# Kernel tuning notes

Hardware: AMD Instinct MI355X
Metric: run time of the kernel (lower is better)

Reference implementation:

```python
import jax, jax.numpy as jnp
import numpy as np
import math

E = 65536        # neighbor pairs (edges)
NAT = 2048       # atoms
NRAD = 24        # radial basis size
ZETA = [1, 2, 3, 4]
NCOMP = len(ZETA) + 1  # radial components: one 2-body + one per zeta
RCUT = 6.0
NELEM = 94       # one-hot element encoding size
EMB = 16         # species embedding dim


def _tables():
    """Static lxlylz enumeration per zeta: triples with lx+ly+lz = n, n in 0..z,
    multinomial/binomial normalization and (-1)^n lambda sign."""
    f = np.vectorize(math.factorial)
    tabs = []
    for z in ZETA:
        L = []
        for n in range(z + 1):
            for lx in range(n + 1):
                for ly in range(n - lx + 1):
                    L.append((lx, ly, n - lx - ly))
        L = np.array(L, np.int64)              # [K,3]
        nsum = L.sum(1)                        # [K]
        fact_lxlylz = f(L[:, 0]) * f(L[:, 1]) * f(L[:, 2])
        # (nfact/fact_lxlylz) * z!/((z-n)! n!) = z! / ((z-n)! * lx!ly!lz!)
        fact_norm = math.factorial(z) / (f(z - nsum) * fact_lxlylz)
        lam = (-1.0) ** nsum
        tabs.append((jnp.asarray(L, jnp.float32),
                     jnp.asarray(fact_norm, jnp.float32),
                     jnp.asarray(lam, jnp.float32)))
    return tabs

TABS = _tables()


def _forward(rij, Wr1, br1, Wr2, br2, Ws1, bs1, Ws2, bs2,
             Wa1, ba1, Wa2, ba2, Wa3, ba3, first_atom_idx, species_idx):
    nat = species_idx.shape[0]
    r = jnp.linalg.norm(rij, axis=1)                       # [E]
    u = rij / r[:, None]                                   # [E,3] unit vectors
    fc = 0.5 * (jnp.cos(jnp.pi * jnp.minimum(r, RCUT) / RCUT) + 1.0)
    centers = jnp.linspace(0.0, RCUT, NRAD, dtype=jnp.float32)
    width = RCUT / NRAD
    basis = jnp.exp(-((r[:, None] - centers) ** 2) / (2.0 * width * width)) * fc[:, None]  # [E,NRAD]
    # learned radial functions -> [E, NRAD, NCOMP]
    h = jax.nn.silu(basis @ Wr1 + br1)
    radial = jax.nn.silu(h @ Wr2 + br2).reshape(-1, NRAD, NCOMP)
    seg = first_atom_idx
    # two-body descriptor
    feats = [jax.ops.segment_sum(radial[:, :, 0], seg, num_segments=nat)]  # [nat,NRAD]
    for iz, z in enumerate(ZETA):
        L, fnorm, lam = TABS[iz]
        # g_ij over lxlylz combos: prod of powers of unit-vector components
        g_ij = jnp.prod((u[:, None, :] + 1e-12) ** L[None, :, :], axis=-1) * fnorm  # [E,K]
        g = jnp.einsum('er,ek->erk', radial[:, :, iz + 1], g_ij)                    # [E,NRAD,K]
        gi = jax.ops.segment_sum(g, seg, num_segments=nat)                          # [nat,NRAD,K]
        g2 = gi * gi
        norm = 2.0 ** (1.0 - z)
        feats.append(jnp.sum(g2, axis=-1) * norm)          # lambda = +1
        feats.append(jnp.sum(g2 * lam, axis=-1) * norm)    # lambda = -1
    feat = jnp.concatenate(feats, axis=1)                  # [nat, NRAD*(1+2*nzeta)]
    # species embedding and correlation
    onehot = jax.nn.one_hot(species_idx, NELEM, dtype=feat.dtype)
    emb = jax.nn.silu(onehot @ Ws1 + bs1) @ Ws2 + bs2      # [nat,EMB]
    x = (feat[:, :, None] * emb[:, None, :]).reshape(nat, -1)  # [nat, F*EMB]
    h = jax.nn.silu(x @ Wa1 + ba1)
    h = jax.nn.silu(h @ Wa2 + ba2)
    e = h @ Wa3 + ba3                                      # [nat,1] atomic energies
    return jnp.sum(e)                                      # total energy


def setup_inputs() -> dict:
    key = jax.random.key(0)
    ks = jax.random.split(key, 12)
    def w(k, shp):
        return jax.random.normal(k, shp, jnp.float32) / np.float32(np.sqrt(shp[0]))
    F = NRAD * (1 + 2 * len(ZETA)) * EMB  # 3456
    return {
        "rij": jax.random.normal(ks[0], (E, 3), jnp.float32) * 2.0,
        "Wr1": w(ks[1], (NRAD, 64)), "br1": jnp.zeros((64,), jnp.float32),
        "Wr2": w(ks[2], (64, NCOMP * NRAD)), "br2": jnp.zeros((NCOMP * NRAD,), jnp.float32),
        "Ws1": w(ks[3], (NELEM, 32)), "bs1": jnp.zeros((32,), jnp.float32),
        "Ws2": w(ks[4], (32, EMB)), "bs2": jnp.zeros((EMB,), jnp.float32),
        "Wa1": w(ks[5], (F, 256)), "ba1": jnp.zeros((256,), jnp.float32),
        "Wa2": w(ks[6], (256, 128)), "ba2": jnp.zeros((128,), jnp.float32),
        "Wa3": w(ks[7], (128, 1)), "ba3": jnp.zeros((1,), jnp.float32),
        "first_atom_idx": jnp.sort(jax.random.randint(ks[8], (E,), 0, NAT)),
        "species_idx": jax.random.randint(ks[9], (NAT,), 0, NELEM),
    }


def reference(rij, Wr1, br1, Wr2, br2, Ws1, bs1, Ws2, bs2,
              Wa1, ba1, Wa2, ba2, Wa3, ba3, first_atom_idx, species_idx):
    return _forward(rij, Wr1, br1, Wr2, br2, Ws1, bs1, Ws2, bs2,
                    Wa1, ba1, Wa2, ba2, Wa3, ba3, first_atom_idx, species_idx)
```

## Files before the change

kernel.cpp:

```cpp
#include <hip/hip_runtime.h>
#include <math.h>

#define KTOT 69
#define NRADC 24
#define NFEAT 216
#define NELEMC 94
#define EMBC 16
#define H1C 256
#define H2C 128
#define CE 16
#define EPR 20
#define KGN 18
#define GSTR 84
#define GISTR 76

__device__ __constant__ int c_lx[KTOT] = {
  0,0,0,1,
  0,0,0,1,0,0,0,1,1,2,
  0,0,0,1,0,0,0,1,1,2,0,0,0,0,1,1,1,2,2,3,
  0,0,0,1,0,0,0,1,1,2,0,0,0,0,1,1,1,2,2,3,0,0,0,0,0,1,1,1,1,2,2,2,3,3,4};
__device__ __constant__ int c_ly[KTOT] = {
  0,0,1,0,
  0,0,1,0,0,1,2,0,1,0,
  0,0,1,0,0,1,2,0,1,0,0,1,2,3,0,1,2,0,1,0,
  0,0,1,0,0,1,2,0,1,0,0,1,2,3,0,1,2,0,1,0,0,1,2,3,4,0,1,2,3,0,1,2,0,1,0};
__device__ __constant__ int c_lz[KTOT] = {
  0,1,0,0,
  0,1,0,0,2,1,0,1,0,0,
  0,1,0,0,2,1,0,1,0,0,3,2,1,0,2,1,0,1,0,0,
  0,1,0,0,2,1,0,1,0,0,3,2,1,0,2,1,0,1,0,0,4,3,2,1,0,3,2,1,0,2,1,0,1,0,0};
__device__ __constant__ float c_fn[KTOT] = {
  1,1,1,1,
  1,2,2,2,1,2,1,2,2,1,
  1,3,3,3,3,6,3,6,6,3,1,3,3,1,3,6,3,3,3,1,
  1,4,4,4,6,12,6,12,12,6,4,12,12,4,12,24,12,12,12,4,
  1,4,6,4,1,4,12,12,4,6,12,6,4,4,1};
__device__ __constant__ float c_lam[KTOT] = {
  1,-1,-1,-1,
  1,-1,-1,-1,1,1,1,1,1,1,
  1,-1,-1,-1,1,1,1,1,1,1,-1,-1,-1,-1,-1,-1,-1,-1,-1,-1,
  1,-1,-1,-1,1,1,1,1,1,1,-1,-1,-1,-1,-1,-1,-1,-1,-1,-1,
  1,1,1,1,1,1,1,1,1,1,1,1,1,1,1};
__device__ __constant__ int c_k0[4] = {0,4,14,34};
__device__ __constant__ int c_kn[4] = {4,10,20,35};
__device__ __constant__ float c_zn[4] = {1.0f, 0.5f, 0.25f, 0.125f};
__device__ __constant__ int c_zidg[KGN] = {0, 1,1,1, 2,2,2,2,2, 3,3,3,3,3,3,3,3,3};

__device__ __forceinline__ float silu(float x) { return x / (1.0f + expf(-x)); }
__device__ __forceinline__ float4 silu4(float4 v) {
  v.x = silu(v.x); v.y = silu(v.y); v.z = silu(v.z); v.w = silu(v.w); return v;
}
__device__ __forceinline__ void fma4(float4& a, float s, const float4 w) {
  a.x += s * w.x; a.y += s * w.y; a.z += s * w.z; a.w += s * w.w;
}
__device__ __forceinline__ void fma44(float4& a, const float4 x, const float4 y) {
  a.x += x.x * y.x; a.y += x.y * y.y; a.z += x.z * y.z; a.w += x.w * y.w;
}
__device__ __forceinline__ float hsum4(const float4 v) { return (v.x + v.y) + (v.z + v.w); }
__device__ __forceinline__ float powsel(int l, float p, float p2, float p3, float p4) {
  float v = 1.0f;
  v = l >= 1 ? p : v;
  v = l >= 2 ? p2 : v;
  v = l >= 3 ? p3 : v;
  v = l >= 4 ? p4 : v;
  return v;
}

__global__ void k_bounds(const int* __restrict__ fai, int* __restrict__ bounds,
                         int E, int nat) {
  int e = blockIdx.x * blockDim.x + threadIdx.x;
  if (e >= E) return;
  int f = fai[e];
  int fp = (e == 0) ? -1 : fai[e - 1];
  for (int a = fp + 1; a <= f; ++a) bounds[a] = e;
  if (e == E - 1)
    for (int a = f + 1; a <= nat; ++a) bounds[a] = E;
}

template <int NQ>
__device__ __forceinline__ void edge_layer2(
    const float* __restrict__ s_h, const float* __restrict__ Wr2,
    const float* __restrict__ br2, float4* __restrict__ radial4,
    int e, int og, int eg, int E) {
  float4 acc[NQ];
  const float4* b2 = (const float4*)(br2 + og * 32);
  #pragma unroll
  for (int q = 0; q < NQ; ++q) acc[q] = b2[q];
  #pragma unroll 2
  for (int j = 0; j < 64; ++j) {
    float hv = s_h[e * 65 + j];
    const float4* w = (const float4*)(Wr2 + j * 120 + og * 32);
    #pragma unroll
    for (int q = 0; q < NQ; ++q) fma4(acc[q], hv, w[q]);
  }
  if (eg < E) {
    #pragma unroll
    for (int q = 0; q < NQ; ++q)
      radial4[(size_t)(og * 8 + q) * E + eg] = silu4(acc[q]);
  }
}

__global__ __launch_bounds__(256) void k_edge(
    const float* __restrict__ rij,
    const float* __restrict__ Wr1, const float* __restrict__ br1,
    const float* __restrict__ Wr2, const float* __restrict__ br2,
    float4* __restrict__ radial4, int E) {
  __shared__ float s_bas[64 * 25];
  __shared__ float s_h[64 * 65];
  const int tid = threadIdx.x;
  const int e = tid & 63;
  const int og = __builtin_amdgcn_readfirstlane(tid >> 6);
  const int eg = blockIdx.x * 64 + e;

  {
    float x = 0.0f, y = 0.0f, z = 0.0f;
    if (eg < E) { x = rij[eg * 3 + 0]; y = rij[eg * 3 + 1]; z = rij[eg * 3 + 2]; }
    float r = sqrtf(x * x + y * y + z * z);
    float rc = fminf(r, 6.0f);
    float fcv = (eg < E)
        ? 0.5f * (cosf(3.14159265358979323846f * rc * (1.0f / 6.0f)) + 1.0f)
        : 0.0f;
    #pragma unroll
    for (int t = 0; t < 6; ++t) {
      int m = og * 6 + t;
      float d = r - (6.0f / 23.0f) * (float)m;
      s_bas[e * 25 + m] = expf(-8.0f * d * d) * fcv;
    }
  }
  __syncthreads();

  {
    const float4* b1 = (const float4*)(br1 + og * 16);
    float4 acc[4] = {b1[0], b1[1], b1[2], b1[3]};
    #pragma unroll 4
    for (int m = 0; m < NRADC; ++m) {
      float b = s_bas[e * 25 + m];
      const float4* w = (const float4*)(Wr1 + m * 64 + og * 16);
      #pragma unroll
      for (int q = 0; q < 4; ++q) fma4(acc[q], b, w[q]);
    }
    #pragma unroll
    for (int q = 0; q < 4; ++q) {
      float4 v = silu4(acc[q]);
      float* dst = &s_h[e * 65 + og * 16 + 4 * q];
      dst[0] = v.x; dst[1] = v.y; dst[2] = v.z; dst[3] = v.w;
    }
  }
  __syncthreads();

  if (og < 3) edge_layer2<8>(s_h, Wr2, br2, radial4, e, og, eg, E);
  else        edge_layer2<6>(s_h, Wr2, br2, radial4, e, og, eg, E);
}

__global__ __launch_bounds__(256) void k_atom(
    const float* __restrict__ rij,
    const float4* __restrict__ radial4,
    const int* __restrict__ bounds,
    float* __restrict__ feat, int E) {
  const int a = blockIdx.x;
  const int tid = threadIdx.x;
  __shared__ __align__(16) float s_radT[120 * EPR];
  __shared__ __align__(16) float s_gijT[KGN * GSTR];
  __shared__ __align__(16) float s_gi[NRADC * GISTR];
  __shared__ float s_feat[NFEAT];

  const int start = bounds[a];
  const int end = bounds[a + 1];

  const bool is_tile = tid < 216;
  const int eh = is_tile ? (tid / 108) : 0;
  const int tile = is_tile ? (tid % 108) : 0;
  const int rg = tile % 6;
  const int kg = tile / 6;
  const int zz = c_zidg[kg];
  const int comp0 = rg * 20 + 1 + zz;
  const bool is_2b = (tid >= 216 && tid < 240);
  const int rad2b = tid - 216;

  if (tid < 60) {
    int rr = tid / EPR, e = tid % EPR;
    int fkg = rr < 2 ? 3 : 17;
    int fj = rr < 2 ? 2 + rr : 3;
    s_gijT[fkg * GSTR + fj * EPR + e] = 0.0f;
  }

  float4 acc[4][4];
  #pragma unroll
  for (int i = 0; i < 4; ++i)
    #pragma unroll
    for (int j = 0; j < 4; ++j) acc[i][j] = make_float4(0, 0, 0, 0);
  float4 acc2b = make_float4(0, 0, 0, 0);

  for (int c0 = start; c0 < end; c0 += CE) {
    const int ne = min(CE, end - c0);
    for (int idx = tid; idx < 30 * CE; idx += 256) {
      int o4 = idx >> 4;
      int e = idx & 15;
      float4 v = make_float4(0, 0, 0, 0);
      if (e < ne) v = radial4[(size_t)o4 * E + (c0 + e)];
      int c = o4 * 4;
      s_radT[(c + 0) * EPR + e] = v.x;
      s_radT[(c + 1) * EPR + e] = v.y;
      s_radT[(c + 2) * EPR + e] = v.z;
      s_radT[(c + 3) * EPR + e] = v.w;
    }
    {
      int e = tid >> 4, sub = tid & 15;
      int eg = c0 + e;
      bool ev = e < ne;
      float x = 1.0f, y = 0.0f, z3 = 0.0f;
      if (ev) { x = rij[eg * 3 + 0]; y = rij[eg * 3 + 1]; z3 = rij[eg * 3 + 2]; }
      float r = sqrtf(x * x + y * y + z3 * z3);
      float inv = 1.0f / r;
      float px = x * inv + 1e-12f, py = y * inv + 1e-12f, pz = z3 * inv + 1e-12f;
      float p2x = px * px, p3x = p2x * px, p4x = p2x * p2x;
      float p2y = py * py, p3y = p2y * py, p4y = p2y * p2y;
      float p2z = pz * pz, p3z = p2z * pz, p4z = p2z * p2z;
      int kstart = sub < 5 ? sub * 5 : 25 + (sub - 5) * 4;
      int kcnt = sub < 5 ? 5 : 4;
      for (int t = 0; t < kcnt; ++t) {
        int k = kstart + t;
        float g = powsel(c_lx[k], px, p2x, p3x, p4x) *
                  powsel(c_ly[k], py, p2y, p3y, p4y) *
                  powsel(c_lz[k], pz, p2z, p3z, p4z) * c_fn[k];
        if (!ev) g = 0.0f;
        int prow = k + (k < 14 ? 0 : 2);
        s_gijT[(prow >> 2) * GSTR + (prow & 3) * EPR + e] = g;
      }
    }
    __syncthreads();
    if (is_tile) {
      #pragma unroll
      for (int s = 0; s < 2; ++s) {
        int e0 = eh * 8 + s * 4;
        float4 gg[4];
        #pragma unroll
        for (int j = 0; j < 4; ++j)
          gg[j] = *(const float4*)&s_gijT[kg * GSTR + j * EPR + e0];
        #pragma unroll
        for (int i = 0; i < 4; ++i) {
          float4 rr = *(const float4*)&s_radT[(comp0 + 5 * i) * EPR + e0];
          #pragma unroll
          for (int j = 0; j < 4; ++j) fma44(acc[i][j], rr, gg[j]);
        }
      }
    }
    if (is_2b) {
      #pragma unroll
      for (int e0 = 0; e0 < 16; e0 += 4) {
        float4 v = *(const float4*)&s_radT[(rad2b * 5) * EPR + e0];
        acc2b.x += v.x; acc2b.y += v.y; acc2b.z += v.z; acc2b.w += v.w;
      }
    }
    __syncthreads();
  }

  float4 hs[4];
  #pragma unroll
  for (int i = 0; i < 4; ++i)
    hs[i] = make_float4(hsum4(acc[i][0]), hsum4(acc[i][1]),
                        hsum4(acc[i][2]), hsum4(acc[i][3]));
  if (is_tile && eh == 0) {
    #pragma unroll
    for (int i = 0; i < 4; ++i)
      *(float4*)&s_gi[(rg * 4 + i) * GISTR + kg * 4] = hs[i];
  }
  if (is_2b) s_feat[rad2b] = hsum4(acc2b);
  __syncthreads();
  if (is_tile && eh == 1) {
    #pragma unroll
    for (int i = 0; i < 4; ++i) {
      float4 v = *(const float4*)&s_gi[(rg * 4 + i) * GISTR + kg * 4];
      v.x += hs[i].x; v.y += hs[i].y; v.z += hs[i].z; v.w += hs[i].w;
      *(float4*)&s_gi[(rg * 4 + i) * GISTR + kg * 4] = v;
    }
  }
  __syncthreads();

  if (tid < 192) {
    int zb = tid / NRADC;
    int rad = tid - zb * NRADC;
    int z = zb >> 1;
    bool neg = zb & 1;
    int k0 = c_k0[z], kn = c_kn[z];
    float s = 0.0f;
    for (int k = k0; k < k0 + kn; ++k) {
      int prow = k + (k < 14 ? 0 : 2);
      float g = s_gi[rad * GISTR + prow];
      float g2 = g * g;
      s += neg ? g2 * c_lam[k] : g2;
    }
    s_feat[NRADC + zb * NRADC + rad] = s * c_zn[z];
  }
  __syncthreads();
  if (tid < NFEAT) feat[(size_t)a * NFEAT + tid] = s_feat[tid];
}

__global__ void k_emb(const float* __restrict__ Ws1, const float* __restrict__ bs1,
                      const float* __restrict__ Ws2, const float* __restrict__ bs2,
                      float* __restrict__ emb) {
  int s = blockIdx.x, t = threadIdx.x;
  __shared__ float hh[32];
  if (t < 32) hh[t] = silu(Ws1[s * 32 + t] + bs1[t]);
  __syncthreads();
  if (t < EMBC) {
    float acc = bs2[t];
    #pragma unroll
    for (int c = 0; c < 32; ++c) acc += hh[c] * Ws2[c * EMBC + t];
    emb[s * EMBC + t] = acc;
  }
}

__global__ __launch_bounds__(256) void k_B(const float* __restrict__ Wa1,
                                           const float* __restrict__ emb,
                                           float* __restrict__ B) {
  const int i = blockIdx.x;
  const int o = threadIdx.x;
  __shared__ float s_emb[NELEMC * EMBC];
  for (int idx = o; idx < NELEMC * EMBC; idx += 256) s_emb[idx] = emb[idx];
  float w[EMBC];
  #pragma unroll
  for (int j = 0; j < EMBC; ++j) w[j] = Wa1[(size_t)(i * EMBC + j) * H1C + o];
  __syncthreads();
  for (int s = 0; s < NELEMC; ++s) {
    float acc = 0.0f;
    #pragma unroll
    for (int j = 0; j < EMBC; ++j) acc += s_emb[s * EMBC + j] * w[j];
    B[((size_t)s * NFEAT + i) * H1C + o] = acc;
  }
}

__global__ void k_sort(const int* __restrict__ sp, int* __restrict__ order, int nat) {
  __shared__ int cnt[NELEMC];
  __shared__ int off[NELEMC];
  int t = threadIdx.x;
  for (int i = t; i < NELEMC; i += 256) cnt[i] = 0;
  __syncthreads();
  for (int a = t; a < nat; a += 256) atomicAdd(&cnt[sp[a]], 1);
  __syncthreads();
  if (t == 0) { int run = 0; for (int s = 0; s < NELEMC; ++s) { off[s] = run; run += cnt[s]; } }
  __syncthreads();
  for (int a = t; a < nat; a += 256) { int pos = atomicAdd(&off[sp[a]], 1); order[pos] = a; }
}

__global__ __launch_bounds__(256) void k_mlp(
    const float* __restrict__ feat, const float* __restrict__ B,
    const float* __restrict__ ba1, const float* __restrict__ Wa2,
    const float* __restrict__ ba2, const float* __restrict__ Wa3,
    const float* __restrict__ ba3, const int* __restrict__ order,
    const int* __restrict__ sp, float* __restrict__ e_out, int nat) {
  const int nb = gridDim.x;
  int rank = blockIdx.x;
  if ((nb & 7) == 0) rank = (blockIdx.x & 7) * (nb >> 3) + (blockIdx.x >> 3);
  const int a = order[rank];
  const int s = sp[a];
  const int t = threadIdx.x;
  __shared__ float s_feat[NFEAT];
  __shared__ float s_h1[H1C];
  __shared__ float s_red[H2C];
  if (t < NFEAT) s_feat[t] = feat[(size_t)a * NFEAT + t];
  __syncthreads();
  {
    double a0 = (double)ba1[t], a1 = 0.0;
    const float* Bp = B + (size_t)s * NFEAT * H1C + t;
    #pragma unroll 4
    for (int i = 0; i < NFEAT; i += 2) {
      a0 += (double)s_feat[i] * (double)Bp[(size_t)i * H1C];
      a1 += (double)s_feat[i + 1] * (double)Bp[(size_t)(i + 1) * H1C];
    }
    s_h1[t] = silu((float)(a0 + a1));
  }
  __syncthreads();
  if (t < H2C) {
    double a0 = (double)ba2[t], a1 = 0.0;
    #pragma unroll 4
    for (int j = 0; j < H1C; j += 2) {
      a0 += (double)s_h1[j] * (double)Wa2[j * H2C + t];
      a1 += (double)s_h1[j + 1] * (double)Wa2[(j + 1) * H2C + t];
    }
    float h2 = silu((float)(a0 + a1));
    s_red[t] = h2 * Wa3[t];
  }
  __syncthreads();
  if (t < 64) {
    float v = s_red[t] + s_red[t + 64];
    for (int o = 32; o; o >>= 1) v += __shfl_down(v, o, 64);
    if (t == 0) e_out[a] = v + ba3[0];
  }
}

__global__ void k_reduce(const float* __restrict__ e_in, float* __restrict__ out, int nat) {
  int t = threadIdx.x;
  double acc = 0.0;
  for (int i = t; i < nat; i += 256) acc += (double)e_in[i];
  for (int o = 32; o; o >>= 1) acc += __shfl_down(acc, o, 64);
  __shared__ double s_par[4];
  if ((t & 63) == 0) s_par[t >> 6] = acc;
  __syncthreads();
  if (t == 0) out[0] = (float)(s_par[0] + s_par[1] + s_par[2] + s_par[3]);
}

extern "C" void kernel_launch(void* const* d_in, const int* in_sizes, int n_in,
                              void* d_out, int out_size, void* d_ws, size_t ws_size,
                              hipStream_t stream) {
  const float* rij = (const float*)d_in[0];
  const float* Wr1 = (const float*)d_in[1];
  const float* br1 = (const float*)d_in[2];
  const float* Wr2 = (const float*)d_in[3];
  const float* br2 = (const float*)d_in[4];
  const float* Ws1 = (const float*)d_in[5];
  const float* bs1 = (const float*)d_in[6];
  const float* Ws2 = (const float*)d_in[7];
  const float* bs2 = (const float*)d_in[8];
  const float* Wa1 = (const float*)d_in[9];
  const float* ba1 = (const float*)d_in[10];
  const float* Wa2 = (const float*)d_in[11];
  const float* ba2 = (const float*)d_in[12];
  const float* Wa3 = (const float*)d_in[13];
  const float* ba3 = (const float*)d_in[14];
  const int* fai = (const int*)d_in[15];
  const int* spc = (const int*)d_in[16];

  const int E = in_sizes[0] / 3;
  const int nat = in_sizes[16];

  float* ws = (float*)d_ws;
  size_t off = 0;
  float* radial = ws + off; off += (size_t)E * 120;
  float* feat = ws + off;   off += (size_t)nat * NFEAT;
  float* emb = ws + off;    off += (size_t)NELEMC * EMBC;
  float* Bm = ws + off;     off += (size_t)NELEMC * NFEAT * H1C;
  float* e_ws = ws + off;   off += (size_t)nat;
  int* order = (int*)(ws + off); off += (size_t)nat;
  int* bounds = (int*)(ws + off);

  k_bounds<<<(E + 255) / 256, 256, 0, stream>>>(fai, bounds, E, nat);
  k_edge<<<(E + 63) / 64, 256, 0, stream>>>(rij, Wr1, br1, Wr2, br2, (float4*)radial, E);
  k_atom<<<nat, 256, 0, stream>>>(rij, (const float4*)radial, bounds, feat, E);
  k_emb<<<NELEMC, 64, 0, stream>>>(Ws1, bs1, Ws2, bs2, emb);
  k_B<<<NFEAT, 256, 0, stream>>>(Wa1, emb, Bm);
  k_sort<<<1, 256, 0, stream>>>(spc, order, nat);
  k_mlp<<<nat, 256, 0, stream>>>(feat, Bm, ba1, Wa2, ba2, Wa3, ba3, order, spc, e_ws, nat);
  k_reduce<<<1, 256, 0, stream>>>(e_ws, (float*)d_out, nat);
}
```

Before: 231.3 us.

## Fuse edge MLP into per-atom kernel, merge prep kernels, warp-per-atom final MLP

The radial MLP now runs inside the per-atom kernel on 16-edge chunks, so the E×120 radial intermediate is never written to or read back from global memory. The bounds, species-sort, embedding and B-matrix setup kernels are merged into one multi-role launch to cut launch count. The atom MLP is rewritten so each wavefront handles one atom with float4 float32 accumulation in place of double. This adds per-chunk syncs and recomputation in the atom kernel and changes accumulation precision.

```diff
diff --git a/kernel.cpp b/kernel.cpp
--- a/kernel.cpp
+++ b/kernel.cpp
@@ -66,99 +66,81 @@
   return v;
 }
 
-__global__ void k_bounds(const int* __restrict__ fai, int* __restrict__ bounds,
-                         int E, int nat) {
-  int e = blockIdx.x * blockDim.x + threadIdx.x;
-  if (e >= E) return;
-  int f = fai[e];
-  int fp = (e == 0) ? -1 : fai[e - 1];
-  for (int a = fp + 1; a <= f; ++a) bounds[a] = e;
-  if (e == E - 1)
-    for (int a = f + 1; a <= nat; ++a) bounds[a] = E;
-}
-
-template <int NQ>
-__device__ __forceinline__ void edge_layer2(
-    const float* __restrict__ s_h, const float* __restrict__ Wr2,
-    const float* __restrict__ br2, float4* __restrict__ radial4,
-    int e, int og, int eg, int E) {
-  float4 acc[NQ];
-  const float4* b2 = (const float4*)(br2 + og * 32);
-  #pragma unroll
-  for (int q = 0; q < NQ; ++q) acc[q] = b2[q];
-  #pragma unroll 2
-  for (int j = 0; j < 64; ++j) {
-    float hv = s_h[e * 65 + j];
-    const float4* w = (const float4*)(Wr2 + j * 120 + og * 32);
+__global__ __launch_bounds__(256) void k_prep(
+    const int* __restrict__ fai, const int* __restrict__ spc,
+    const float* __restrict__ Ws1, const float* __restrict__ bs1,
+    const float* __restrict__ Ws2, const float* __restrict__ bs2,
+    const float* __restrict__ Wa1,
+    int* __restrict__ bounds, int* __restrict__ order,
+    float* __restrict__ B, int E, int nat, int nbB) {
+  const int blk = blockIdx.x;
+  const int tid = threadIdx.x;
+  __shared__ float s_hh[NELEMC * 32];
+  __shared__ float s_emb[NELEMC * EMBC];
+  __shared__ int s_cnt[NELEMC];
+  __shared__ int s_off[NELEMC];
+
+  if (blk < nbB) {
+    int e = blk * 256 + tid;
+    if (e < E) {
+      int f = fai[e];
+      int fp = (e == 0) ? -1 : fai[e - 1];
+      for (int a = fp + 1; a <= f; ++a) bounds[a] = e;
+      if (e == E - 1)
+        for (int a = f + 1; a <= nat; ++a) bounds[a] = E;
+    }
+  } else if (blk == nbB) {
+    for (int i = tid; i < NELEMC; i += 256) s_cnt[i] = 0;
+    __syncthreads();
+    for (int a = tid; a < nat; a += 256) atomicAdd(&s_cnt[spc[a]], 1);
+    __syncthreads();
+    if (tid == 0) {
+      int run = 0;
+      for (int s = 0; s < NELEMC; ++s) { s_off[s] = run; run += s_cnt[s]; }
+    }
+    __syncthreads();
+    for (int a = tid; a < nat; a += 256) {
+      int pos = atomicAdd(&s_off[spc[a]], 1);
+      order[pos] = a;
+    }
+  } else {
+    const int i = blk - nbB - 1;
+    const int o = tid;
+    for (int idx = tid; idx < NELEMC * 32; idx += 256) {
+      int s = idx >> 5, c = idx & 31;
+      s_hh[idx] = silu(Ws1[s * 32 + c] + bs1[c]);
+    }
+    __syncthreads();
+    for (int idx = tid; idx < NELEMC * EMBC; idx += 256) {
+      int s = idx >> 4, j = idx & 15;
+      float acc = bs2[j];
+      #pragma unroll
+      for (int c = 0; c < 32; ++c) acc += s_hh[s * 32 + c] * Ws2[c * EMBC + j];
+      s_emb[idx] = acc;
+    }
+    __syncthreads();
+    float w[EMBC];
     #pragma unroll
-    for (int q = 0; q < NQ; ++q) fma4(acc[q], hv, w[q]);
-  }
-  if (eg < E) {
-    #pragma unroll
-    for (int q = 0; q < NQ; ++q)
-      radial4[(size_t)(og * 8 + q) * E + eg] = silu4(acc[q]);
-  }
-}
-
-__global__ __launch_bounds__(256) void k_edge(
+    for (int j = 0; j < EMBC; ++j) w[j] = Wa1[(size_t)(i * EMBC + j) * H1C + o];
+    for (int s = 0; s < NELEMC; ++s) {
+      float acc = 0.0f;
+      #pragma unroll
+      for (int j = 0; j < EMBC; ++j) acc += s_emb[s * EMBC + j] * w[j];
+      B[((size_t)s * NFEAT + i) * H1C + o] = acc;
+    }
+  }
+}
+
+__global__ __launch_bounds__(256) void k_fused(
     const float* __restrict__ rij,
     const float* __restrict__ Wr1, const float* __restrict__ br1,
     const float* __restrict__ Wr2, const float* __restrict__ br2,
-    float4* __restrict__ radial4, int E) {
-  __shared__ float s_bas[64 * 25];
-  __shared__ float s_h[64 * 65];
-  const int tid = threadIdx.x;
-  const int e = tid & 63;
-  const int og = __builtin_amdgcn_readfirstlane(tid >> 6);
-  const int eg = blockIdx.x * 64 + e;
-
-  {
-    float x = 0.0f, y = 0.0f, z = 0.0f;
-    if (eg < E) { x = rij[eg * 3 + 0]; y = rij[eg * 3 + 1]; z = rij[eg * 3 + 2]; }
-    float r = sqrtf(x * x + y * y + z * z);
-    float rc = fminf(r, 6.0f);
-    float fcv = (eg < E)
-        ? 0.5f * (cosf(3.14159265358979323846f * rc * (1.0f / 6.0f)) + 1.0f)
-        : 0.0f;
-    #pragma unroll
-    for (int t = 0; t < 6; ++t) {
-      int m = og * 6 + t;
-      float d = r - (6.0f / 23.0f) * (float)m;
-      s_bas[e * 25 + m] = expf(-8.0f * d * d) * fcv;
-    }
-  }
-  __syncthreads();
-
-  {
-    const float4* b1 = (const float4*)(br1 + og * 16);
-    float4 acc[4] = {b1[0], b1[1], b1[2], b1[3]};
-    #pragma unroll 4
-    for (int m = 0; m < NRADC; ++m) {
-      float b = s_bas[e * 25 + m];
-      const float4* w = (const float4*)(Wr1 + m * 64 + og * 16);
-      #pragma unroll
-      for (int q = 0; q < 4; ++q) fma4(acc[q], b, w[q]);
-    }
-    #pragma unroll
-    for (int q = 0; q < 4; ++q) {
-      float4 v = silu4(acc[q]);
-      float* dst = &s_h[e * 65 + og * 16 + 4 * q];
-      dst[0] = v.x; dst[1] = v.y; dst[2] = v.z; dst[3] = v.w;
-    }
-  }
-  __syncthreads();
-
-  if (og < 3) edge_layer2<8>(s_h, Wr2, br2, radial4, e, og, eg, E);
-  else        edge_layer2<6>(s_h, Wr2, br2, radial4, e, og, eg, E);
-}
-
-__global__ __launch_bounds__(256) void k_atom(
-    const float* __restrict__ rij,
-    const float4* __restrict__ radial4,
     const int* __restrict__ bounds,
     float* __restrict__ feat, int E) {
   const int a = blockIdx.x;
   const int tid = threadIdx.x;
+  __shared__ float s_bas[16 * 25];
+  __shared__ __align__(16) float s_h[16 * 68];
   __shared__ __align__(16) float s_radT[120 * EPR];
   __shared__ __align__(16) float s_gijT[KGN * GSTR];
   __shared__ __align__(16) float s_gi[NRADC * GISTR];
@@ -167,21 +149,35 @@
   const int start = bounds[a];
   const int end = bounds[a + 1];
 
+  const int e = tid & 15;
+  const int sub = tid >> 4;
+
   const bool is_tile = tid < 216;
-  const int eh = is_tile ? (tid / 108) : 0;
-  const int tile = is_tile ? (tid % 108) : 0;
+  const int eh = (tid < 216) ? (tid / 108) : 0;
+  const int tile = (tid < 216) ? (tid % 108) : 0;
   const int rg = tile % 6;
   const int kg = tile / 6;
-  const int zz = c_zidg[kg];
-  const int comp0 = rg * 20 + 1 + zz;
+  const int comp0 = rg * 20 + 1 + c_zidg[kg];
   const bool is_2b = (tid >= 216 && tid < 240);
   const int rad2b = tid - 216;
 
+  const int kstart = sub < 5 ? sub * 5 : 25 + (sub - 5) * 4;
+  const int kcnt = sub < 5 ? 5 : 4;
+  int t_pk[5], t_addr[5]; float t_fn[5];
+  #pragma unroll
+  for (int t = 0; t < 5; ++t) {
+    int k = (t < kcnt) ? kstart + t : 0;
+    t_pk[t] = c_lx[k] | (c_ly[k] << 8) | (c_lz[k] << 16);
+    t_fn[t] = c_fn[k];
+    int prow = k + (k < 14 ? 0 : 2);
+    t_addr[t] = (prow >> 2) * GSTR + (prow & 3) * EPR + e;
+  }
+
   if (tid < 60) {
-    int rr = tid / EPR, e = tid % EPR;
+    int rr = tid / EPR, ec = tid % EPR;
     int fkg = rr < 2 ? 3 : 17;
     int fj = rr < 2 ? 2 + rr : 3;
-    s_gijT[fkg * GSTR + fj * EPR + e] = 0.0f;
+    s_gijT[fkg * GSTR + fj * EPR + ec] = 0.0f;
   }
 
   float4 acc[4][4];
@@ -193,39 +189,72 @@
 
   for (int c0 = start; c0 < end; c0 += CE) {
     const int ne = min(CE, end - c0);
-    for (int idx = tid; idx < 30 * CE; idx += 256) {
-      int o4 = idx >> 4;
-      int e = idx & 15;
-      float4 v = make_float4(0, 0, 0, 0);
-      if (e < ne) v = radial4[(size_t)o4 * E + (c0 + e)];
-      int c = o4 * 4;
-      s_radT[(c + 0) * EPR + e] = v.x;
-      s_radT[(c + 1) * EPR + e] = v.y;
-      s_radT[(c + 2) * EPR + e] = v.z;
-      s_radT[(c + 3) * EPR + e] = v.w;
-    }
+    const bool ev = (e < ne);
+    const int eg = c0 + e;
+    float x = 0.0f, y = 0.0f, z = 0.0f;
+    if (ev) { x = rij[eg * 3 + 0]; y = rij[eg * 3 + 1]; z = rij[eg * 3 + 2]; }
+    const float r = sqrtf(x * x + y * y + z * z);
     {
-      int e = tid >> 4, sub = tid & 15;
-      int eg = c0 + e;
-      bool ev = e < ne;
-      float x = 1.0f, y = 0.0f, z3 = 0.0f;
-      if (ev) { x = rij[eg * 3 + 0]; y = rij[eg * 3 + 1]; z3 = rij[eg * 3 + 2]; }
-      float r = sqrtf(x * x + y * y + z3 * z3);
+      float fcv = ev ? 0.5f * (cosf(3.14159265358979323846f * fminf(r, 6.0f) *
+                                    (1.0f / 6.0f)) + 1.0f)
+                     : 0.0f;
+      float d = r - (6.0f / 23.0f) * (float)sub;
+      s_bas[e * 25 + sub] = expf(-8.0f * d * d) * fcv;
+      if (sub < 8) {
+        float d2 = r - (6.0f / 23.0f) * (float)(16 + sub);
+        s_bas[e * 25 + 16 + sub] = expf(-8.0f * d2 * d2) * fcv;
+      }
+    }
+    __syncthreads();
+    {
+      float4 hacc = *(const float4*)(br1 + sub * 4);
+      #pragma unroll 8
+      for (int m = 0; m < NRADC; ++m) {
+        float b = s_bas[e * 25 + m];
+        float4 w = *(const float4*)(Wr1 + m * 64 + sub * 4);
+        fma4(hacc, b, w);
+      }
+      *(float4*)&s_h[e * 68 + sub * 4] = silu4(hacc);
+    }
+    __syncthreads();
+    if (sub < 15) {
+      const int o0 = sub * 8;
+      float4 aA = *(const float4*)(br2 + o0);
+      float4 aB = *(const float4*)(br2 + o0 + 4);
+      #pragma unroll 4
+      for (int j = 0; j < 64; ++j) {
+        float hv = s_h[e * 68 + j];
+        float4 wA = *(const float4*)(Wr2 + j * 120 + o0);
+        float4 wB = *(const float4*)(Wr2 + j * 120 + o0 + 4);
+        fma4(aA, hv, wA);
+        fma4(aB, hv, wB);
+      }
+      aA = silu4(aA); aB = silu4(aB);
+      if (!ev) { aA = make_float4(0, 0, 0, 0); aB = make_float4(0, 0, 0, 0); }
+      s_radT[(o0 + 0) * EPR + e] = aA.x;
+      s_radT[(o0 + 1) * EPR + e] = aA.y;
+      s_radT[(o0 + 2) * EPR + e] = aA.z;
+      s_radT[(o0 + 3) * EPR + e] = aA.w;
+      s_radT[(o0 + 4) * EPR + e] = aB.x;
+      s_radT[(o0 + 5) * EPR + e] = aB.y;
+      s_radT[(o0 + 6) * EPR + e] = aB.z;
+      s_radT[(o0 + 7) * EPR + e] = aB.w;
+    }
+    {
       float inv = 1.0f / r;
-      float px = x * inv + 1e-12f, py = y * inv + 1e-12f, pz = z3 * inv + 1e-12f;
+      float px = x * inv + 1e-12f, py = y * inv + 1e-12f, pz = z * inv + 1e-12f;
       float p2x = px * px, p3x = p2x * px, p4x = p2x * p2x;
       float p2y = py * py, p3y = p2y * py, p4y = p2y * p2y;
       float p2z = pz * pz, p3z = p2z * pz, p4z = p2z * p2z;
-      int kstart = sub < 5 ? sub * 5 : 25 + (sub - 5) * 4;
-      int kcnt = sub < 5 ? 5 : 4;
-      for (int t = 0; t < kcnt; ++t) {
-        int k = kstart + t;
-        float g = powsel(c_lx[k], px, p2x, p3x, p4x) *
-                  powsel(c_ly[k], py, p2y, p3y, p4y) *
-                  powsel(c_lz[k], pz, p2z, p3z, p4z) * c_fn[k];
-        if (!ev) g = 0.0f;
-        int prow = k + (k < 14 ? 0 : 2);
-        s_gijT[(prow >> 2) * GSTR + (prow & 3) * EPR + e] = g;
+      #pragma unroll
+      for (int t = 0; t < 5; ++t) {
+        if (t < kcnt) {
+          int pk = t_pk[t];
+          float g = powsel(pk & 0xff, px, p2x, p3x, p4x) *
+                    powsel((pk >> 8) & 0xff, py, p2y, p3y, p4y) *
+                    powsel(pk >> 16, pz, p2z, p3z, p4z) * t_fn[t];
+          s_gijT[t_addr[t]] = ev ? g : 0.0f;
+        }
       }
     }
     __syncthreads();
@@ -296,53 +325,6 @@
   if (tid < NFEAT) feat[(size_t)a * NFEAT + tid] = s_feat[tid];
 }
 
-__global__ void k_emb(const float* __restrict__ Ws1, const float* __restrict__ bs1,
-                      const float* __restrict__ Ws2, const float* __restrict__ bs2,
-                      float* __restrict__ emb) {
-  int s = blockIdx.x, t = threadIdx.x;
-  __shared__ float hh[32];
-  if (t < 32) hh[t] = silu(Ws1[s * 32 + t] + bs1[t]);
-  __syncthreads();
-  if (t < EMBC) {
-    float acc = bs2[t];
-    #pragma unroll
-    for (int c = 0; c < 32; ++c) acc += hh[c] * Ws2[c * EMBC + t];
-    emb[s * EMBC + t] = acc;
-  }
-}
-
-__global__ __launch_bounds__(256) void k_B(const float* __restrict__ Wa1,
-                                           const float* __restrict__ emb,
-                                           float* __restrict__ B) {
-  const int i = blockIdx.x;
-  const int o = threadIdx.x;
-  __shared__ float s_emb[NELEMC * EMBC];
-  for (int idx = o; idx < NELEMC * EMBC; idx += 256) s_emb[idx] = emb[idx];
-  float w[EMBC];
-  #pragma unroll
-  for (int j = 0; j < EMBC; ++j) w[j] = Wa1[(size_t)(i * EMBC + j) * H1C + o];
-  __syncthreads();
-  for (int s = 0; s < NELEMC; ++s) {
-    float acc = 0.0f;
-    #pragma unroll
-    for (int j = 0; j < EMBC; ++j) acc += s_emb[s * EMBC + j] * w[j];
-    B[((size_t)s * NFEAT + i) * H1C + o] = acc;
-  }
-}
-
-__global__ void k_sort(const int* __restrict__ sp, int* __restrict__ order, int nat) {
-  __shared__ int cnt[NELEMC];
-  __shared__ int off[NELEMC];
-  int t = threadIdx.x;
-  for (int i = t; i < NELEMC; i += 256) cnt[i] = 0;
-  __syncthreads();
-  for (int a = t; a < nat; a += 256) atomicAdd(&cnt[sp[a]], 1);
-  __syncthreads();
-  if (t == 0) { int run = 0; for (int s = 0; s < NELEMC; ++s) { off[s] = run; run += cnt[s]; } }
-  __syncthreads();
-  for (int a = t; a < nat; a += 256) { int pos = atomicAdd(&off[sp[a]], 1); order[pos] = a; }
-}
-
 __global__ __launch_bounds__(256) void k_mlp(
     const float* __restrict__ feat, const float* __restrict__ B,
     const float* __restrict__ ba1, const float* __restrict__ Wa2,
@@ -350,42 +332,51 @@
     const float* __restrict__ ba3, const int* __restrict__ order,
     const int* __restrict__ sp, float* __restrict__ e_out, int nat) {
   const int nb = gridDim.x;
-  int rank = blockIdx.x;
-  if ((nb & 7) == 0) rank = (blockIdx.x & 7) * (nb >> 3) + (blockIdx.x >> 3);
+  int blk = blockIdx.x;
+  if ((nb & 7) == 0) blk = (blockIdx.x & 7) * (nb >> 3) + (blockIdx.x >> 3);
+  const int w = threadIdx.x >> 6;
+  const int l = threadIdx.x & 63;
+  const int rank = blk * 4 + w;
+  if (rank >= nat) return;
   const int a = order[rank];
   const int s = sp[a];
-  const int t = threadIdx.x;
-  __shared__ float s_feat[NFEAT];
-  __shared__ float s_h1[H1C];
-  __shared__ float s_red[H2C];
-  if (t < NFEAT) s_feat[t] = feat[(size_t)a * NFEAT + t];
+  __shared__ __align__(16) float s_f[4][220];
+  __shared__ __align__(16) float s_h1[4][260];
+
+  if (l < 54) {
+    float4 v = *(const float4*)(feat + (size_t)a * NFEAT + l * 4);
+    *(float4*)&s_f[w][l * 4] = v;
+  }
   __syncthreads();
   {
-    double a0 = (double)ba1[t], a1 = 0.0;
-    const float* Bp = B + (size_t)s * NFEAT * H1C + t;
-    #pragma unroll 4
+    float4 a0 = *(const float4*)(ba1 + l * 4);
+    float4 a1 = make_float4(0, 0, 0, 0);
+    const float* Bp = B + (size_t)s * NFEAT * H1C + l * 4;
+    #pragma unroll 8
     for (int i = 0; i < NFEAT; i += 2) {
-      a0 += (double)s_feat[i] * (double)Bp[(size_t)i * H1C];
-      a1 += (double)s_feat[i + 1] * (double)Bp[(size_t)(i + 1) * H1C];
-    }
-    s_h1[t] = silu((float)(a0 + a1));
-  }
-  __syncthreads();
-  if (t < H2C) {
-    double a0 = (double)ba2[t], a1 = 0.0;
-    #pragma unroll 4
-    for (int j = 0; j < H1C; j += 2) {
-      a0 += (double)s_h1[j] * (double)Wa2[j * H2C + t];
-      a1 += (double)s_h1[j + 1] * (double)Wa2[(j + 1) * H2C + t];
-    }
-    float h2 = silu((float)(a0 + a1));
-    s_red[t] = h2 * Wa3[t];
-  }
-  __syncthreads();
-  if (t < 64) {
-    float v = s_red[t] + s_red[t + 64];
-    for (int o = 32; o; o >>= 1) v += __shfl_down(v, o, 64);
-    if (t == 0) e_out[a] = v + ba3[0];
+      float4 b0 = *(const float4*)(Bp + (size_t)i * H1C);
+      float4 b1 = *(const float4*)(Bp + (size_t)(i + 1) * H1C);
+      fma4(a0, s_f[w][i], b0);
+      fma4(a1, s_f[w][i + 1], b1);
+    }
+    a0.x += a1.x; a0.y += a1.y; a0.z += a1.z; a0.w += a1.w;
+    *(float4*)&s_h1[w][l * 4] = silu4(a0);
+  }
+  __syncthreads();
+  {
+    float a0 = ba2[2 * l], a1 = ba2[2 * l + 1];
+    #pragma unroll 8
+    for (int j = 0; j < H1C; ++j) {
+      float hv = s_h1[w][j];
+      float2 wv = *(const float2*)(Wa2 + j * H2C + 2 * l);
+      a0 += hv * wv.x;
+      a1 += hv * wv.y;
+    }
+    float2 w3 = *(const float2*)(Wa3 + 2 * l);
+    float part = silu(a0) * w3.x + silu(a1) * w3.y;
+    #pragma unroll
+    for (int o = 32; o; o >>= 1) part += __shfl_down(part, o, 64);
+    if (l == 0) e_out[a] = part + ba3[0];
   }
 }
 
@@ -426,20 +417,17 @@
 
   float* ws = (float*)d_ws;
   size_t off = 0;
-  float* radial = ws + off; off += (size_t)E * 120;
-  float* feat = ws + off;   off += (size_t)nat * NFEAT;
-  float* emb = ws + off;    off += (size_t)NELEMC * EMBC;
-  float* Bm = ws + off;     off += (size_t)NELEMC * NFEAT * H1C;
-  float* e_ws = ws + off;   off += (size_t)nat;
+  float* feat = ws + off;  off += (size_t)nat * NFEAT;
+  float* Bm = ws + off;    off += (size_t)NELEMC * NFEAT * H1C;
+  float* e_ws = ws + off;  off += (size_t)nat;
   int* order = (int*)(ws + off); off += (size_t)nat;
   int* bounds = (int*)(ws + off);
 
-  k_bounds<<<(E + 255) / 256, 256, 0, stream>>>(fai, bounds, E, nat);
-  k_edge<<<(E + 63) / 64, 256, 0, stream>>>(rij, Wr1, br1, Wr2, br2, (float4*)radial, E);
-  k_atom<<<nat, 256, 0, stream>>>(rij, (const float4*)radial, bounds, feat, E);
-  k_emb<<<NELEMC, 64, 0, stream>>>(Ws1, bs1, Ws2, bs2, emb);
-  k_B<<<NFEAT, 256, 0, stream>>>(Wa1, emb, Bm);
-  k_sort<<<1, 256, 0, stream>>>(spc, order, nat);
-  k_mlp<<<nat, 256, 0, stream>>>(feat, Bm, ba1, Wa2, ba2, Wa3, ba3, order, spc, e_ws, nat);
+  const int nbB = (E + 255) / 256;
+  k_prep<<<nbB + 1 + NFEAT, 256, 0, stream>>>(fai, spc, Ws1, bs1, Ws2, bs2, Wa1,
+                                              bounds, order, Bm, E, nat, nbB);
+  k_fused<<<nat, 256, 0, stream>>>(rij, Wr1, br1, Wr2, br2, bounds, feat, E);
+  k_mlp<<<(nat + 3) / 4, 256, 0, stream>>>(feat, Bm, ba1, Wa2, ba2, Wa3, ba3,
+                                           order, spc, e_ws, nat);
   k_reduce<<<1, 256, 0, stream>>>(e_ws, (float*)d_out, nat);
 }
```

Result: slower. 291.1 us (+25.9%).
